# Optimization experiments

Hardware: AMD Instinct MI355X
Metric: run time of the kernel (lower is better)

## Reference

```python
import jax, jax.numpy as jnp
import numpy as np

N_NODES = 50000
N_EDGES = 800000
IN_CH, HID_CH, OUT_CH = 128, 256, 256
N_LAYERS = 3


def setup_inputs() -> dict:
    key = jax.random.key(0)
    ks = jax.random.split(key, 9)
    x = jax.random.normal(ks[0], (N_NODES, IN_CH), dtype=jnp.float32)
    edge_index = jax.random.randint(ks[1], (2, N_EDGES), 0, N_NODES, dtype=jnp.int32)
    # Linear params, Kaiming-ish scale
    W1 = jax.random.normal(ks[2], (IN_CH, HID_CH), dtype=jnp.float32) / np.float32(np.sqrt(IN_CH))
    b1 = jnp.zeros((HID_CH,), jnp.float32)
    W2 = jax.random.normal(ks[3], (HID_CH, HID_CH), dtype=jnp.float32) / np.float32(np.sqrt(HID_CH))
    b2 = jnp.zeros((HID_CH,), jnp.float32)
    W3 = jax.random.normal(ks[4], (HID_CH, OUT_CH), dtype=jnp.float32) / np.float32(np.sqrt(HID_CH))
    b3 = jnp.zeros((OUT_CH,), jnp.float32)
    # learnable eps per GINConv (train_eps=True); small nonzero values for a nontrivial test
    eps = jax.random.normal(ks[5], (N_LAYERS,), dtype=jnp.float32) * 0.01
    return {"x": x, "edge_index": edge_index, "W1": W1, "b1": b1,
            "W2": W2, "b2": b2, "W3": W3, "b3": b3, "eps": eps}


def _gin_conv(x, src, dst, eps, W, b):
    # sum aggregation over incoming edges: agg[i] = sum_{(j->i)} x[j]
    agg = jax.ops.segment_sum(x[src], dst, num_segments=N_NODES)
    h = (1.0 + eps) * x + agg
    return h @ W + b


def reference(x, edge_index, W1, b1, W2, b2, W3, b3, eps):
    src, dst = edge_index[0], edge_index[1]
    # layers 0..L-2: conv -> relu -> dropout (identity in eval mode)
    h = jax.nn.relu(_gin_conv(x, src, dst, eps[0], W1, b1))
    h = jax.nn.relu(_gin_conv(h, src, dst, eps[1], W2, b2))
    # final layer: no relu
    out = _gin_conv(h, src, dst, eps[2], W3, b3)
    return out
```

## Files before the change

### kernel.cpp

```cpp
#include <hip/hip_runtime.h>


typedef __attribute__((ext_vector_type(8))) short short8;
typedef __attribute__((ext_vector_type(4))) float f32x4;

__device__ inline unsigned short f2bf(float f) {
    union { float f; unsigned u; } v; v.f = f;
    unsigned r = v.u + 0x7fffu + ((v.u >> 16) & 1u);
    return (unsigned short)(r >> 16);
}
__device__ inline float bflo(unsigned u) { return __uint_as_float(u << 16); }
__device__ inline float bfhi(unsigned u) { return __uint_as_float(u & 0xffff0000u); }

__device__ __forceinline__ void gload_lds16(const unsigned short* g, unsigned short* l) {
    __builtin_amdgcn_global_load_lds(
        (const __attribute__((address_space(1))) unsigned int*)g,
        (__attribute__((address_space(3))) unsigned int*)l,
        16, 0, 0);
}

#define ACC8(v) { acc[0]+=bflo(v.x); acc[1]+=bfhi(v.x); acc[2]+=bflo(v.y); acc[3]+=bfhi(v.y); \
                  acc[4]+=bflo(v.z); acc[5]+=bfhi(v.z); acc[6]+=bflo(v.w); acc[7]+=bfhi(v.w); }

__global__ __launch_bounds__(256) void prep_kernel(
    const float* __restrict__ x, const int* __restrict__ dst,
    const float* __restrict__ W1, const float* __restrict__ W2,
    const float* __restrict__ W3,
    unsigned short* __restrict__ xb, int* __restrict__ cnt,
    unsigned short* __restrict__ Ws1, unsigned short* __restrict__ Ws2,
    unsigned short* __restrict__ Ws3, int M, int nE)
{
    const int i  = blockIdx.x * 256 + threadIdx.x;
    const int nx = M * 16;
    if (i < nx) {
        const float4* xf = reinterpret_cast<const float4*>(x);
        float4 a = xf[2*i], b = xf[2*i + 1];
        uint4 o;
        o.x = (unsigned)f2bf(a.x) | ((unsigned)f2bf(a.y) << 16);
        o.y = (unsigned)f2bf(a.z) | ((unsigned)f2bf(a.w) << 16);
        o.z = (unsigned)f2bf(b.x) | ((unsigned)f2bf(b.y) << 16);
        o.w = (unsigned)f2bf(b.z) | ((unsigned)f2bf(b.w) << 16);
        const int node = i >> 4;
        const int c0   = (i & 15) * 8;
        const int cs   = c0 >> 4;
        const size_t idx = (size_t)cs * M * 16 + (size_t)node * 16 + (c0 & 15);
        *reinterpret_cast<uint4*>(xb + idx) = o;
    } else if (i < nx + nE) {
        atomicAdd(&cnt[dst[i - nx]], 1);
    } else {
        int j = i - nx - nE;
        const float* W; unsigned short* D;
        if (j < 32768)       { W = W1; D = Ws1; }
        else if (j < 98304)  { W = W2; D = Ws2; j -= 32768; }
        else if (j < 163840) { W = W3; D = Ws3; j -= 98304; }
        else return;
        const int k = j >> 8, n = j & 255;
        D[((size_t)(k >> 3) * 256 + n) * 8 + (k & 7)] = f2bf(W[(size_t)k * 256 + n]);
    }
}


__global__ __launch_bounds__(1024) void scan1_kernel(
    const int* __restrict__ cnt, int* __restrict__ excl,
    int* __restrict__ bsum, int n)
{
    __shared__ int sh[1024];
    const int tid = threadIdx.x;
    const int i = blockIdx.x * 1024 + tid;
    int v = (i < n) ? cnt[i] : 0;
    sh[tid] = v;
    __syncthreads();
    #pragma unroll
    for (int off = 1; off < 1024; off <<= 1) {
        int t = (tid >= off) ? sh[tid - off] : 0;
        __syncthreads();
        sh[tid] += t;
        __syncthreads();
    }
    if (i < n) excl[i] = sh[tid] - v;
    if (tid == 1023) bsum[blockIdx.x] = sh[1023];
}

__global__ __launch_bounds__(1024) void scan3_kernel(
    const int* __restrict__ excl, const int* __restrict__ bsum,
    int* __restrict__ row_start, int* __restrict__ cursor,
    int n, int nE, int nbl)
{
    __shared__ int sb[64];
    const int tid = threadIdx.x;
    if (tid < 64) sb[tid] = (tid < nbl) ? bsum[tid] : 0;
    __syncthreads();
    #pragma unroll
    for (int off = 1; off < 64; off <<= 1) {
        int v = 0;
        if (tid < 64 && tid >= off) v = sb[tid - off];
        __syncthreads();
        if (tid < 64) sb[tid] += v;
        __syncthreads();
    }
    const int boff = sb[blockIdx.x] - bsum[blockIdx.x];
    const int i = blockIdx.x * 1024 + tid;
    if (i < n) {
        int v = excl[i] + boff;
        row_start[i] = v;
        cursor[i] = v;
    }
    if (i == 0) row_start[n] = nE;
}

__global__ __launch_bounds__(256) void build_adj_kernel(
    const int* __restrict__ src, const int* __restrict__ dst,
    int* __restrict__ cursor, int* __restrict__ adj, int nE)
{
    int e = blockIdx.x * 256 + threadIdx.x;
    if (e < nE) {
        int p = atomicAdd(&cursor[dst[e]], 1);
        adj[p] = src[e];
    }
}


template <int CIN>
__global__ __launch_bounds__(256) void agg_sliced(
    const unsigned short* __restrict__ Xcs,
    const int* __restrict__ row_start, const int* __restrict__ adj,
    const float* __restrict__ eps_arr, int layer,
    unsigned short* __restrict__ H, int M)
{
    constexpr int SC  = CIN / 8;
    constexpr int U4  = SC / 8;
    constexpr int NPB = 256 / U4;

    const int cs   = blockIdx.x & 7;
    const int grp  = blockIdx.x >> 3;
    const int node = grp * NPB + (threadIdx.x / U4);
    const int c8   = threadIdx.x & (U4 - 1);
    if (node >= M) return;

    const uint4* __restrict__ X4 =
        reinterpret_cast<const uint4*>(Xcs) + (size_t)cs * M * U4;

    float acc[8] = {};
    const int s0 = row_start[node];
    const int s1 = row_start[node + 1];

    int j = s0;
    for (; j + 3 < s1; j += 4) {
        int a0 = adj[j], a1 = adj[j+1], a2 = adj[j+2], a3 = adj[j+3];
        uint4 v0 = X4[(size_t)a0 * U4 + c8];
        uint4 v1 = X4[(size_t)a1 * U4 + c8];
        uint4 v2 = X4[(size_t)a2 * U4 + c8];
        uint4 v3 = X4[(size_t)a3 * U4 + c8];
        ACC8(v0); ACC8(v1); ACC8(v2); ACC8(v3);
    }
    for (; j < s1; ++j) {
        uint4 v = X4[(size_t)adj[j] * U4 + c8];
        ACC8(v);
    }

    const uint4 xv = X4[(size_t)node * U4 + c8];
    const float epsv = 1.0f + eps_arr[layer];
    float o[8];
    o[0] = epsv * bflo(xv.x) + acc[0]; o[1] = epsv * bfhi(xv.x) + acc[1];
    o[2] = epsv * bflo(xv.y) + acc[2]; o[3] = epsv * bfhi(xv.y) + acc[3];
    o[4] = epsv * bflo(xv.z) + acc[4]; o[5] = epsv * bfhi(xv.z) + acc[5];
    o[6] = epsv * bflo(xv.w) + acc[6]; o[7] = epsv * bfhi(xv.w) + acc[7];

    uint4 ov;
    ov.x = (unsigned)f2bf(o[0]) | ((unsigned)f2bf(o[1]) << 16);
    ov.y = (unsigned)f2bf(o[2]) | ((unsigned)f2bf(o[3]) << 16);
    ov.z = (unsigned)f2bf(o[4]) | ((unsigned)f2bf(o[5]) << 16);
    ov.w = (unsigned)f2bf(o[6]) | ((unsigned)f2bf(o[7]) << 16);
    *reinterpret_cast<uint4*>(H + (size_t)node * CIN + cs * SC + c8 * 8) = ov;
}


template <int CIN, int RELU, int OUTMODE>
__global__ __launch_bounds__(256) void gemm_tiled(
    const unsigned short* __restrict__ H, const unsigned short* __restrict__ Wsub,
    const float* __restrict__ bias, void* __restrict__ out, int M)
{
    constexpr int S = CIN / 32;

    __shared__ __align__(16) unsigned short As[2][4][64][8];

    const int t    = threadIdx.x;
    const int bm   = blockIdx.x * 64;
    const int w    = t >> 6, lane = t & 63;
    const int lr   = lane & 15, ko = lane >> 4;

    const int srow = t & 63;
    const int skb  = t >> 6;
    const unsigned short* aG = H + (size_t)(bm + srow) * CIN + skb * 8;

    f32x4 acc[4][4];
    #pragma unroll
    for (int fn = 0; fn < 4; ++fn) {
        const float bb = bias[w*64 + fn*16 + lr];
        #pragma unroll
        for (int fm = 0; fm < 4; ++fm) {
            acc[fm][fn][0] = bb; acc[fm][fn][1] = bb;
            acc[fm][fn][2] = bb; acc[fm][fn][3] = bb;
        }
    }

    gload_lds16(aG, &As[0][skb][srow][0]);

    int cur = 0;
    for (int s = 0; s < S; ++s) {
        __syncthreads();
        if (s + 1 < S)
            gload_lds16(aG + (s+1)*32, &As[cur ^ 1][skb][srow][0]);

        short8 af[4], bf8[4];
        #pragma unroll
        for (int fm = 0; fm < 4; ++fm)
            af[fm] = *reinterpret_cast<const short8*>(&As[cur][ko][fm*16 + lr][0]);
        #pragma unroll
        for (int fn = 0; fn < 4; ++fn)
            bf8[fn] = *reinterpret_cast<const short8*>(
                Wsub + ((size_t)(s*4 + ko) * 256 + w*64 + fn*16 + lr) * 8);
        #pragma unroll
        for (int fm = 0; fm < 4; ++fm)
            #pragma unroll
            for (int fn = 0; fn < 4; ++fn)
                acc[fm][fn] = __builtin_amdgcn_mfma_f32_16x16x32_bf16(
                    af[fm], bf8[fn], acc[fm][fn], 0, 0, 0);

        cur ^= 1;
    }

    #pragma unroll
    for (int fm = 0; fm < 4; ++fm) {
        #pragma unroll
        for (int fn = 0; fn < 4; ++fn) {
            const int col = w*64 + fn*16 + lr;
            #pragma unroll
            for (int r = 0; r < 4; ++r) {
                const int row = bm + fm*16 + ko*4 + r;
                if (row < M) {
                    float v = acc[fm][fn][r];
                    if (RELU) v = fmaxf(v, 0.f);
                    if (OUTMODE == 1) {
                        ((unsigned short*)out)[(size_t)(col >> 5) * M * 32
                                               + (size_t)row * 32 + (col & 31)] = f2bf(v);
                    } else {
                        ((float*)out)[(size_t)row * 256 + col] = v;
                    }
                }
            }
        }
    }
}


extern "C" void kernel_launch(void* const* d_in, const int* in_sizes, int n_in,
                              void* d_out, int out_size, void* d_ws, size_t ws_size,
                              hipStream_t stream)
{
    const float* x   = (const float*)d_in[0];
    const int*   ei  = (const int*)  d_in[1];
    const float* W1  = (const float*)d_in[2];
    const float* b1  = (const float*)d_in[3];
    const float* W2  = (const float*)d_in[4];
    const float* b2  = (const float*)d_in[5];
    const float* W3  = (const float*)d_in[6];
    const float* b3  = (const float*)d_in[7];
    const float* eps = (const float*)d_in[8];

    const int M  = in_sizes[0] / 128;
    const int nE = in_sizes[1] / 2;
    const int Mp = ((M + 63) / 64) * 64;
    const int* srcI = ei;
    const int* dstI = ei + nE;

    char* p = (char*)d_ws;
    unsigned short* xb_cs = (unsigned short*)p; p += (size_t)M  * 128 * 2;
    unsigned short* Arow  = (unsigned short*)p; p += (size_t)Mp * 256 * 2;
    unsigned short* s_cs  = (unsigned short*)p; p += (size_t)M  * 256 * 2;
    unsigned short* Ws1   = (unsigned short*)p; p += (size_t)128 * 256 * 2;
    unsigned short* Ws2   = (unsigned short*)p; p += (size_t)256 * 256 * 2;
    unsigned short* Ws3   = (unsigned short*)p; p += (size_t)256 * 256 * 2;
    int* cnt       = (int*)p; p += (size_t)M * 4;
    int* excl      = (int*)p; p += (size_t)M * 4;
    int* bsum      = (int*)p; p += 64 * 4;
    int* row_start = (int*)p; p += (size_t)(M + 2) * 4;
    int* cursor    = (int*)p; p += (size_t)M * 4;
    int* adj       = (int*)p; p += (size_t)nE * 4;

    const int nbl = (M + 1023) / 1024;

    hipMemsetAsync(cnt, 0, (size_t)M * sizeof(int), stream);
    {
        const int total = M * 16 + nE + 163840;
        prep_kernel<<<(total + 255) / 256, 256, 0, stream>>>(
            x, dstI, W1, W2, W3, xb_cs, cnt, Ws1, Ws2, Ws3, M, nE);
    }
    scan1_kernel<<<nbl, 1024, 0, stream>>>(cnt, excl, bsum, M);
    scan3_kernel<<<nbl, 1024, 0, stream>>>(excl, bsum, row_start, cursor, M, nE, nbl);
    build_adj_kernel<<<(nE + 255) / 256, 256, 0, stream>>>(srcI, dstI, cursor, adj, nE);

    const int ablk1 = 8 * ((M + 127) / 128);
    const int ablk2 = 8 * ((M + 63) / 64);
    const int gblk  = Mp / 64;

    agg_sliced<128><<<ablk1, 256, 0, stream>>>(xb_cs, row_start, adj, eps, 0, Arow, M);
    gemm_tiled<128, 1, 1><<<gblk, 256, 0, stream>>>(Arow, Ws1, b1, s_cs, M);

    agg_sliced<256><<<ablk2, 256, 0, stream>>>(s_cs, row_start, adj, eps, 1, Arow, M);
    gemm_tiled<256, 1, 1><<<gblk, 256, 0, stream>>>(Arow, Ws2, b2, s_cs, M);

    agg_sliced<256><<<ablk2, 256, 0, stream>>>(s_cs, row_start, adj, eps, 2, Arow, M);
    gemm_tiled<256, 0, 0><<<gblk, 256, 0, stream>>>(Arow, Ws3, b3, d_out, M);
}
```

Baseline: 301.5 us.

## Build CSR adjacency via two-pass bucketed binning instead of global atomics

Replaces the per-edge global atomicAdd scatter into the CSR adjacency with a two-stage bucket sort. Edges are first binned by destination range into 256 buckets, using shared-memory histograms and one global atomic per bucket per block. Each bucket is then scattered locally with LDS atomics. This aims to cut global atomic contention and make the writes more local, at the cost of an extra pass and an extra pair buffer. Packing dst and src into 16 bits each assumes node ids fit in 16 bits, which 50000 does, and 256 buckets of 196 nodes covers at most 50176 nodes.

Measured after the change: 274.0 us. 1.1x faster.

```diff
diff --git a/kernel.cpp b/kernel.cpp
--- a/kernel.cpp
+++ b/kernel.cpp
@@ -3,6 +3,9 @@
 
 typedef __attribute__((ext_vector_type(8))) short short8;
 typedef __attribute__((ext_vector_type(4))) float f32x4;
+
+#define NBUK   256
+#define BNODES 196
 
 __device__ inline unsigned short f2bf(float f) {
     union { float f; unsigned u; } v; v.f = f;
@@ -83,7 +86,7 @@
 
 __global__ __launch_bounds__(1024) void scan3_kernel(
     const int* __restrict__ excl, const int* __restrict__ bsum,
-    int* __restrict__ row_start, int* __restrict__ cursor,
+    int* __restrict__ row_start, int* __restrict__ gcur,
     int n, int nE, int nbl)
 {
     __shared__ int sb[64];
@@ -103,22 +106,67 @@
     if (i < n) {
         int v = excl[i] + boff;
         row_start[i] = v;
-        cursor[i] = v;
+        if ((i % BNODES) == 0) gcur[i / BNODES] = v;
     }
     if (i == 0) row_start[n] = nE;
 }
 
-__global__ __launch_bounds__(256) void build_adj_kernel(
+__global__ __launch_bounds__(256) void binA_kernel(
     const int* __restrict__ src, const int* __restrict__ dst,
-    int* __restrict__ cursor, int* __restrict__ adj, int nE)
-{
-    int e = blockIdx.x * 256 + threadIdx.x;
-    if (e < nE) {
-        int p = atomicAdd(&cursor[dst[e]], 1);
-        adj[p] = src[e];
-    }
-}
-
+    int* __restrict__ gcur, unsigned* __restrict__ pair_buf, int nE)
+{
+    __shared__ int lhist[NBUK];
+    __shared__ int lbase[NBUK];
+    const int t = threadIdx.x;
+    lhist[t] = 0;
+    __syncthreads();
+
+    const int e0 = blockIdx.x * 4096;
+    int d[16], s[16], r[16];
+    #pragma unroll
+    for (int i = 0; i < 16; ++i) {
+        const int e = e0 + i * 256 + t;
+        if (e < nE) {
+            d[i] = dst[e];
+            s[i] = src[e];
+            r[i] = atomicAdd(&lhist[d[i] / BNODES], 1);
+        }
+    }
+    __syncthreads();
+    lbase[t] = lhist[t] ? atomicAdd(&gcur[t], lhist[t]) : 0;
+    __syncthreads();
+    #pragma unroll
+    for (int i = 0; i < 16; ++i) {
+        const int e = e0 + i * 256 + t;
+        if (e < nE)
+            pair_buf[lbase[d[i] / BNODES] + r[i]] =
+                ((unsigned)d[i] << 16) | (unsigned)s[i];
+    }
+}
+
+__global__ __launch_bounds__(256) void binB_kernel(
+    const unsigned* __restrict__ pair_buf, const int* __restrict__ row_start,
+    int* __restrict__ adj, int M)
+{
+    __shared__ int lcur[BNODES];
+    const int b   = blockIdx.x;
+    const int nb0 = b * BNODES;
+    const int nb1 = min(nb0 + BNODES, M);
+    const int nn  = nb1 - nb0;
+    const int t   = threadIdx.x;
+    if (nn <= 0) return;
+    for (int i = t; i < nn; i += 256) lcur[i] = row_start[nb0 + i];
+    __syncthreads();
+    const int p0 = row_start[nb0];
+    const int p1 = row_start[nb1];
+    for (int p = p0 + t; p < p1; p += 256) {
+        const unsigned pr = pair_buf[p];
+        const int dn = (int)(pr >> 16);
+        const int sn = (int)(pr & 0xFFFFu);
+        const int pos = atomicAdd(&lcur[dn - nb0], 1);
+        adj[pos] = sn;
+    }
+}
 
 template <int CIN>
 __global__ __launch_bounds__(256) void agg_sliced(
@@ -173,7 +221,6 @@
     ov.w = (unsigned)f2bf(o[6]) | ((unsigned)f2bf(o[7]) << 16);
     *reinterpret_cast<uint4*>(H + (size_t)node * CIN + cs * SC + c8 * 8) = ov;
 }
-
 
 template <int CIN, int RELU, int OUTMODE>
 __global__ __launch_bounds__(256) void gemm_tiled(
@@ -284,8 +331,9 @@
     int* cnt       = (int*)p; p += (size_t)M * 4;
     int* excl      = (int*)p; p += (size_t)M * 4;
     int* bsum      = (int*)p; p += 64 * 4;
+    int* gcur      = (int*)p; p += NBUK * 4;
     int* row_start = (int*)p; p += (size_t)(M + 2) * 4;
-    int* cursor    = (int*)p; p += (size_t)M * 4;
+    unsigned* pair_buf = (unsigned*)p; p += (size_t)nE * 4;
     int* adj       = (int*)p; p += (size_t)nE * 4;
 
     const int nbl = (M + 1023) / 1024;
@@ -297,8 +345,9 @@
             x, dstI, W1, W2, W3, xb_cs, cnt, Ws1, Ws2, Ws3, M, nE);
     }
     scan1_kernel<<<nbl, 1024, 0, stream>>>(cnt, excl, bsum, M);
-    scan3_kernel<<<nbl, 1024, 0, stream>>>(excl, bsum, row_start, cursor, M, nE, nbl);
-    build_adj_kernel<<<(nE + 255) / 256, 256, 0, stream>>>(srcI, dstI, cursor, adj, nE);
+    scan3_kernel<<<nbl, 1024, 0, stream>>>(excl, bsum, row_start, gcur, M, nE, nbl);
+    binA_kernel<<<(nE + 4095) / 4096, 256, 0, stream>>>(srcI, dstI, gcur, pair_buf, nE);
+    binB_kernel<<<NBUK, 256, 0, stream>>>(pair_buf, row_start, adj, M);
 
     const int ablk1 = 8 * ((M + 127) / 128);
     const int ablk2 = 8 * ((M + 63) / 64);
```
